# Kernel tuning notes

Measured on AMD Instinct MI355X. Metric: run time of the kernel, lower is better.

## Reference

```python
import jax, jax.numpy as jnp
import numpy as np

EPS = 1e-5

def _ln(x):
    m = jnp.mean(x, axis=-1, keepdims=True)
    v = jnp.mean((x - m) ** 2, axis=-1, keepdims=True)
    return (x - m) / jnp.sqrt(v + EPS)

def setup_inputs() -> dict:
    key = jax.random.key(0)
    ks = jax.random.split(key, 6)
    B, S, E, H = 2, 2048, 1024, 16
    sd = 1.0 / np.sqrt(E)
    x = jax.random.normal(ks[0], (B, S, E), dtype=jnp.float32)
    w_in = jax.random.normal(ks[1], (3 * E, E), dtype=jnp.float32) * sd
    w_out = jax.random.normal(ks[2], (E, E), dtype=jnp.float32) * sd
    w_fc = jax.random.normal(ks[3], (4 * E, E), dtype=jnp.float32) * sd
    b_fc = jnp.zeros((4 * E,), dtype=jnp.float32)
    w_proj = jax.random.normal(ks[4], (E, 4 * E), dtype=jnp.float32) * (1.0 / np.sqrt(4 * E))
    b_proj = jnp.zeros((E,), dtype=jnp.float32)
    return {"x": x, "w_in": w_in, "w_out": w_out, "w_fc": w_fc,
            "b_fc": b_fc, "w_proj": w_proj, "b_proj": b_proj}

def reference(x, w_in, w_out, w_fc, b_fc, w_proj, b_proj):
    B, S, E = x.shape
    H = 16
    D = E // H
    h = _ln(x)
    qkv = h @ w_in.T                      # [B,S,3E]
    q, k, v = jnp.split(qkv, 3, axis=-1)
    q = q.reshape(B, S, H, D)
    k = k.reshape(B, S, H, D)
    v = v.reshape(B, S, H, D)
    scale = 1.0 / np.sqrt(D)
    scores = jnp.einsum('bqhd,bkhd->bhqk', q, k) * scale  # [B,H,S,S]
    causal = jnp.tril(jnp.ones((S, S), dtype=bool))
    scores = jnp.where(causal, scores, -jnp.inf)
    attn = jax.nn.softmax(scores, axis=-1)
    o = jnp.einsum('bhqk,bkhd->bqhd', attn, v).reshape(B, S, E)
    attn_out = o @ w_out.T
    x2 = x + attn_out                      # residual 1
    h2 = _ln(x2)
    m = jax.nn.relu(h2 @ w_fc.T + b_fc)    # [B,S,4E]
    return (m @ w_proj.T + b_proj) + x2    # residual 2
```

## Files before the change

### kernel.cpp

```cpp
#include <hip/hip_runtime.h>
#include <stdint.h>

#define AS1 __attribute__((address_space(1)))
#define AS3 __attribute__((address_space(3)))

typedef __bf16 bf8_t __attribute__((ext_vector_type(8)));
typedef float f4_t __attribute__((ext_vector_type(4)));
typedef unsigned short ush;

__device__ __forceinline__ ush f2b(float f) {
  unsigned u = __builtin_bit_cast(unsigned, f);
  u += 0x7fffu + ((u >> 16) & 1u);
  return (ush)(u >> 16);
}
__device__ __forceinline__ void unpack8(uint4 u, float* dst) {
  unsigned a0 = u.x, a1 = u.y, a2 = u.z, a3 = u.w;
  dst[0] = __builtin_bit_cast(float, a0 << 16);
  dst[1] = __builtin_bit_cast(float, a0 & 0xffff0000u);
  dst[2] = __builtin_bit_cast(float, a1 << 16);
  dst[3] = __builtin_bit_cast(float, a1 & 0xffff0000u);
  dst[4] = __builtin_bit_cast(float, a2 << 16);
  dst[5] = __builtin_bit_cast(float, a2 & 0xffff0000u);
  dst[6] = __builtin_bit_cast(float, a3 << 16);
  dst[7] = __builtin_bit_cast(float, a3 & 0xffff0000u);
}

__global__ __launch_bounds__(256) void f2b_all(
    const float* __restrict__ w_in, const float* __restrict__ w_out,
    const float* __restrict__ w_fc, const float* __restrict__ w_proj,
    ush* __restrict__ o_in, ush* __restrict__ o_out,
    ush* __restrict__ o_fc, ush* __restrict__ o_proj) {
  const int blk = blockIdx.x;
  const float* src;
  ush* dst;
  int base;
  if (blk < 3072) { src = w_in; dst = o_in; base = blk; }
  else if (blk < 4096) { src = w_out; dst = o_out; base = blk - 3072; }
  else if (blk < 8192) { src = w_fc; dst = o_fc; base = blk - 4096; }
  else { src = w_proj; dst = o_proj; base = blk - 8192; }
  const int i = (base * 256 + threadIdx.x) * 4;
  float4 v = *(const float4*)(src + i);
  union { ush u[4]; uint2 d; } p;
  p.u[0] = f2b(v.x); p.u[1] = f2b(v.y); p.u[2] = f2b(v.z); p.u[3] = f2b(v.w);
  *(uint2*)(dst + i) = p.d;
}

__global__ __launch_bounds__(256) void ln_kernel(const float* __restrict__ x,
                                                 ush* __restrict__ out) {
  const int row = blockIdx.x, tid = threadIdx.x;
  const float* xr = x + (size_t)row * 1024;
  float4 v = ((const float4*)xr)[tid];
  float s = v.x + v.y + v.z + v.w;
  float q = v.x * v.x + v.y * v.y + v.z * v.z + v.w * v.w;
  for (int o = 32; o; o >>= 1) { s += __shfl_down(s, o); q += __shfl_down(q, o); }
  __shared__ float rs[4], rq[4];
  const int w = tid >> 6;
  if ((tid & 63) == 0) { rs[w] = s; rq[w] = q; }
  __syncthreads();
  s = rs[0] + rs[1] + rs[2] + rs[3];
  q = rq[0] + rq[1] + rq[2] + rq[3];
  const float mean = s * (1.0f / 1024.0f);
  const float var = q * (1.0f / 1024.0f) - mean * mean;
  const float rstd = rsqrtf(var + 1e-5f);
  union { ush u[4]; uint2 d; } p;
  p.u[0] = f2b((v.x - mean) * rstd);
  p.u[1] = f2b((v.y - mean) * rstd);
  p.u[2] = f2b((v.z - mean) * rstd);
  p.u[3] = f2b((v.w - mean) * rstd);
  *(uint2*)(out + (size_t)row * 1024 + tid * 4) = p.d;
}

template <int EPI>
__global__ __launch_bounds__(512, 2) void gemm8p(
    const ush* __restrict__ A, const ush* __restrict__ Bw,
    int M, int N, int K,
    const float* __restrict__ bias, const float* __restrict__ resid,
    float* __restrict__ outF, ush* __restrict__ outB) {
  __shared__ __align__(16) ush lds[65536];
  ush* const LA0 = lds;
  ush* const LA1 = lds + 16384;
  ush* const LB0 = lds + 32768;
  ush* const LB1 = lds + 49152;

  const int tid = threadIdx.x;
  const int wave = tid >> 6, lane = tid & 63;
  const int wm = wave >> 2, wn = wave & 3;
  const int l16 = lane & 15, quad = lane >> 4;
  const int sw = l16 & 7;
  const int bm = blockIdx.x, bn = blockIdx.y;
  const int bmrow = bm * 256, bnrow = bn * 256;
  const int KT = K >> 6;
  const int nit = KT >> 1;
  const int gcs = (((lane & 7) ^ ((lane >> 3) & 7)) << 3);

  auto stage = [&](const ush* __restrict__ gbase, int blkrow, ush* dstbase,
                   int t, int h) {
    const int kt = t & (KT - 1);
#pragma unroll
    for (int i2 = 0; i2 < 2; ++i2) {
      const int rr = h * 128 + (wave * 2 + i2) * 8 + (lane >> 3);
      const ush* g = gbase + (size_t)(blkrow + rr) * K + kt * 64 + gcs;
      __builtin_amdgcn_global_load_lds(
          (const AS1 void*)g,
          (AS3 void*)(dstbase + h * 8192 + (wave * 2 + i2) * 512), 16, 0, 0);
    }
  };

  f4_t acc[8][4];
#pragma unroll
  for (int i = 0; i < 8; ++i)
#pragma unroll
    for (int j = 0; j < 4; ++j) acc[i][j] = (f4_t){0.f, 0.f, 0.f, 0.f};

  stage(A, bmrow, LA0, 0, 0);
  stage(A, bmrow, LA0, 0, 1);
  stage(Bw, bnrow, LB0, 0, 0);
  stage(Bw, bnrow, LB0, 0, 1);
  stage(A, bmrow, LA1, 1, 0);
  asm volatile("s_waitcnt vmcnt(2)" ::: "memory");
  __builtin_amdgcn_s_barrier();

  bf8_t af[4][2], bf[2][2];

  for (int it = 0; it < nit; ++it) {
#pragma unroll
    for (int hf = 0; hf < 2; ++hf) {
      ush* const cA = hf ? LA1 : LA0;
      ush* const cB = hf ? LB1 : LB0;
#pragma unroll
      for (int sub = 0; sub < 4; ++sub) {
        const int p = hf * 4 + sub;
        if (sub == 0) {
#pragma unroll
          for (int m = 0; m < 4; ++m)
#pragma unroll
            for (int kk = 0; kk < 2; ++kk)
              af[m][kk] = *(const bf8_t*)&cA[(wm * 128 + m * 16 + l16) * 64 +
                                            (((kk * 4 + quad) ^ sw) << 3)];
#pragma unroll
          for (int n = 0; n < 2; ++n)
#pragma unroll
            for (int kk = 0; kk < 2; ++kk)
              bf[n][kk] = *(const bf8_t*)&cB[(wn * 64 + n * 16 + l16) * 64 +
                                            (((kk * 4 + quad) ^ sw) << 3)];
        } else if (sub == 1) {
#pragma unroll
          for (int n = 0; n < 2; ++n)
#pragma unroll
            for (int kk = 0; kk < 2; ++kk)
              bf[n][kk] = *(const bf8_t*)&cB[(wn * 64 + (2 + n) * 16 + l16) * 64 +
                                            (((kk * 4 + quad) ^ sw) << 3)];
        } else if (sub == 2) {
#pragma unroll
          for (int m = 0; m < 4; ++m)
#pragma unroll
            for (int kk = 0; kk < 2; ++kk)
              af[m][kk] = *(const bf8_t*)&cA[(wm * 128 + (4 + m) * 16 + l16) * 64 +
                                            (((kk * 4 + quad) ^ sw) << 3)];
#pragma unroll
          for (int n = 0; n < 2; ++n)
#pragma unroll
            for (int kk = 0; kk < 2; ++kk)
              bf[n][kk] = *(const bf8_t*)&cB[(wn * 64 + n * 16 + l16) * 64 +
                                            (((kk * 4 + quad) ^ sw) << 3)];
        } else {
#pragma unroll
          for (int n = 0; n < 2; ++n)
#pragma unroll
            for (int kk = 0; kk < 2; ++kk)
              bf[n][kk] = *(const bf8_t*)&cB[(wn * 64 + (2 + n) * 16 + l16) * 64 +
                                            (((kk * 4 + quad) ^ sw) << 3)];
        }
        if (p == 0) stage(A, bmrow, LA1, 2 * it + 1, 1);
        else if (p == 1) stage(Bw, bnrow, LB1, 2 * it + 1, 0);
        else if (p == 2) stage(Bw, bnrow, LB1, 2 * it + 1, 1);
        else if (p == 3) stage(A, bmrow, LA0, 2 * it + 2, 0);
        else if (p == 4) stage(A, bmrow, LA0, 2 * it + 2, 1);
        else if (p == 5) stage(Bw, bnrow, LB0, 2 * it + 2, 0);
        else if (p == 6) stage(Bw, bnrow, LB0, 2 * it + 2, 1);
        else stage(A, bmrow, LA1, 2 * it + 3, 0);
        if (sub == 3) asm volatile("s_waitcnt vmcnt(2)" ::: "memory");
        __builtin_amdgcn_s_barrier();
        asm volatile("s_waitcnt lgkmcnt(0)" ::: "memory");
        __builtin_amdgcn_sched_barrier(0);
        __builtin_amdgcn_s_setprio(1);
        const int mo = (sub >= 2) ? 4 : 0;
        const int no = (sub & 1) ? 2 : 0;
#pragma unroll
        for (int m = 0; m < 4; ++m)
#pragma unroll
          for (int n = 0; n < 2; ++n)
#pragma unroll
            for (int kk = 0; kk < 2; ++kk)
              acc[mo + m][no + n] = __builtin_amdgcn_mfma_f32_16x16x32_bf16(
                  af[m][kk], bf[n][kk], acc[mo + m][no + n], 0, 0, 0);
        __builtin_amdgcn_s_setprio(0);
        __builtin_amdgcn_s_barrier();
      }
    }
  }

  asm volatile("s_waitcnt vmcnt(0)" ::: "memory");
  __builtin_amdgcn_s_barrier();

  if (EPI == 0 || EPI == 2) {
    ush* eb = lds + wave * 8192;
    float bv[4];
    if (EPI == 2) {
#pragma unroll
      for (int ni = 0; ni < 4; ++ni) bv[ni] = bias[bn * 256 + wn * 64 + ni * 16 + l16];
    }
#pragma unroll
    for (int mi = 0; mi < 8; ++mi)
#pragma unroll
      for (int ni = 0; ni < 4; ++ni)
#pragma unroll
        for (int r = 0; r < 4; ++r) {
          float v = acc[mi][ni][r];
          if (EPI == 2) v = fmaxf(v + bv[ni], 0.0f);
          eb[(mi * 16 + quad * 4 + r) * 64 + ni * 16 + l16] = f2b(v);
        }
    asm volatile("s_waitcnt lgkmcnt(0)" ::: "memory");
#pragma unroll
    for (int j = 0; j < 16; ++j) {
      const int lr = j * 8 + (lane >> 3);
      const int c8 = (lane & 7) * 8;
      uint4 v = *(const uint4*)&eb[lr * 64 + c8];
      *(uint4*)(outB + (size_t)(bm * 256 + wm * 128 + lr) * N + bn * 256 +
                wn * 64 + c8) = v;
    }
  } else {
#pragma unroll
    for (int mi = 0; mi < 8; ++mi)
#pragma unroll
      for (int ni = 0; ni < 4; ++ni) {
        const int gm0 = bm * 256 + wm * 128 + mi * 16 + quad * 4;
        const int gn = bn * 256 + wn * 64 + ni * 16 + l16;
        const float bv = (EPI == 3) ? bias[gn] : 0.0f;
#pragma unroll
        for (int r = 0; r < 4; ++r) {
          const size_t idx = (size_t)(gm0 + r) * N + gn;
          outF[idx] = acc[mi][ni][r] + bv + resid[idx];
        }
      }
  }
}

template <int EPI, int BM, int MINW>
__global__ __launch_bounds__(256, MINW) void gemm_bt(
    const ush* __restrict__ A, const ush* __restrict__ Bw,
    int M, int N, int K,
    const float* __restrict__ bias, const float* __restrict__ resid,
    float* __restrict__ outF, ush* __restrict__ outB) {
  constexpr int MI = BM / 32;
  constexpr int NCH = (BM + 128) / 16;
  constexpr int PC = NCH / 4;
  constexpr int ASZ = BM * 32;
  __shared__ ush lds[2 * ASZ + 2 * 4096];
  const int tid = threadIdx.x;
  const int wave = tid >> 6, lane = tid & 63;
  const int bm = blockIdx.x, bn = blockIdx.y;
  const int wm = (wave & 1) * (BM / 2), wn = (wave >> 1) * 64;
  const int l16 = lane & 15, quad = lane >> 4;
  const int srow = lane >> 2;
  const int scol = (lane & 3) * 8;

  const ush* Abase = A + (size_t)(bm * BM) * K;
  const ush* Bbase = Bw + (size_t)(bn * 128) * K;

  f4_t acc[MI][4];
#pragma unroll
  for (int i = 0; i < MI; ++i)
#pragma unroll
    for (int j = 0; j < 4; ++j) acc[i][j] = (f4_t){0.f, 0.f, 0.f, 0.f};

  const int kiters = K >> 5;

  auto stage = [&](int k0, int buf) {
    const int kk = k0 * 32;
#pragma unroll
    for (int i = 0; i < PC; ++i) {
      const int c = wave * PC + i;
      if (c < BM / 16) {
        const ush* ga = Abase + (size_t)(c * 16 + srow) * K + kk + scol;
        __builtin_amdgcn_global_load_lds((const AS1 void*)ga,
                                         (AS3 void*)(lds + buf * ASZ + c * 512), 16, 0, 0);
      } else {
        const int c2 = c - BM / 16;
        const ush* gb = Bbase + (size_t)(c2 * 16 + srow) * K + kk + scol;
        __builtin_amdgcn_global_load_lds(
            (const AS1 void*)gb, (AS3 void*)(lds + 2 * ASZ + buf * 4096 + c2 * 512), 16, 0, 0);
      }
    }
  };

  stage(0, 0);
  __syncthreads();
  for (int k0 = 0; k0 < kiters; ++k0) {
    const int cur = k0 & 1;
    if (k0 + 1 < kiters) stage(k0 + 1, cur ^ 1);
    bf8_t af[MI], bfr[4];
#pragma unroll
    for (int mi = 0; mi < MI; ++mi)
      af[mi] = *(const bf8_t*)&lds[cur * ASZ + (wm + mi * 16 + l16) * 32 + quad * 8];
#pragma unroll
    for (int ni = 0; ni < 4; ++ni)
      bfr[ni] = *(const bf8_t*)&lds[2 * ASZ + cur * 4096 + (wn + ni * 16 + l16) * 32 + quad * 8];
#pragma unroll
    for (int mi = 0; mi < MI; ++mi)
#pragma unroll
      for (int ni = 0; ni < 4; ++ni)
        acc[mi][ni] =
            __builtin_amdgcn_mfma_f32_16x16x32_bf16(af[mi], bfr[ni], acc[mi][ni], 0, 0, 0);
    __syncthreads();
  }

  if (EPI == 0 || EPI == 2) {
    ush* eb = lds + wave * ASZ;
#pragma unroll
    for (int mi = 0; mi < MI; ++mi)
#pragma unroll
      for (int ni = 0; ni < 4; ++ni) {
        const int gn = bn * 128 + wn + ni * 16 + l16;
        const float bv = (EPI == 2) ? bias[gn] : 0.0f;
#pragma unroll
        for (int r = 0; r < 4; ++r) {
          float v = acc[mi][ni][r] + bv;
          if (EPI == 2) v = fmaxf(v, 0.0f);
          eb[(mi * 16 + quad * 4 + r) * 64 + ni * 16 + l16] = f2b(v);
        }
      }
#pragma unroll
    for (int j = 0; j < BM / 16; ++j) {
      const int lr = j * 8 + (lane >> 3);
      const int c8 = (lane & 7) * 8;
      uint4 v = *(const uint4*)&eb[lr * 64 + c8];
      *(uint4*)(outB + (size_t)(bm * BM + wm + lr) * N + bn * 128 + wn + c8) = v;
    }
  } else {
#pragma unroll
    for (int mi = 0; mi < MI; ++mi) {
#pragma unroll
      for (int ni = 0; ni < 4; ++ni) {
        const int gm0 = bm * BM + wm + mi * 16 + quad * 4;
        const int gn = bn * 128 + wn + ni * 16 + l16;
        const float bv = (EPI == 3) ? bias[gn] : 0.0f;
#pragma unroll
        for (int r = 0; r < 4; ++r) {
          const size_t idx = (size_t)(gm0 + r) * N + gn;
          outF[idx] = acc[mi][ni][r] + bv + resid[idx];
        }
      }
    }
  }
}

__global__ __launch_bounds__(256) void pack_kv(const ush* __restrict__ qkv,
                                               ush* __restrict__ Kp,
                                               ush* __restrict__ Vp) {
  const int lin = blockIdx.x;
  const int kt = lin & 31, h = (lin >> 5) & 15, b = lin >> 9;
  const int tid = threadIdx.x;
  __shared__ ush Vs[64 * 72];
  const size_t rowbase = (size_t)(b * 2048 + kt * 64) * 3072 + h * 64;
  ush* Kt = Kp + (size_t)lin * 4096;
  ush* Vt = Vp + (size_t)lin * 4096;

  const int r0 = tid >> 3, cin = tid & 7;
#pragma unroll
  for (int it = 0; it < 2; ++it) {
    const int r = r0 + it * 32;
    uint4 ku = *(const uint4*)(qkv + rowbase + (size_t)r * 3072 + 1024 + cin * 8);
    float f[8]; unpack8(ku, f);
    union { ush us[8]; uint4 v; } pk;
#pragma unroll
    for (int j = 0; j < 8; ++j) pk.us[j] = f2b(f[j] * 0.125f);
    *(uint4*)(Kt + (size_t)(r * 8 + (cin ^ (r & 7))) * 8) = pk.v;
    uint4 vu = *(const uint4*)(qkv + rowbase + (size_t)r * 3072 + 2048 + cin * 8);
    *(uint4*)&Vs[r * 72 + cin * 8] = vu;
  }
  __syncthreads();
#pragma unroll
  for (int oc2 = 0; oc2 < 2; ++oc2) {
    const int oc = tid * 2 + oc2;
    const int d = oc >> 3, c = oc & 7;
    const int k0 = 8 * (c ^ (d & 7));
    union { ush us[8]; uint4 v; } pk;
#pragma unroll
    for (int j = 0; j < 8; ++j) pk.us[j] = Vs[(k0 + j) * 72 + d];
    *(uint4*)(Vt + (size_t)oc * 8) = pk.v;
  }
}

__global__ __launch_bounds__(256, 4) void attn_kernel(const ush* __restrict__ qkv,
                                                      const ush* __restrict__ Kp,
                                                      const ush* __restrict__ Vp,
                                                      ush* __restrict__ o) {
  const int lin = blockIdx.x;
  const int b = lin & 1, h = (lin >> 1) & 15, tq = lin >> 5;
  const int tid = threadIdx.x;
  const int wave = tid >> 6, lane = tid & 63;
  const int l15 = lane & 15, quad = lane >> 4;

  __shared__ __align__(16) ush Ks[64 * 64];
  __shared__ __align__(16) ush Vt[64 * 64];
  __shared__ __align__(16) ush Ps[64 * 72];

  bf8_t qf[2];
  {
    const int qrow = b * 2048 + tq * 64 + wave * 16 + l15;
#pragma unroll
    for (int s = 0; s < 2; ++s) {
      union { uint4 u; bf8_t v; } pk;
      pk.u = *(const uint4*)(qkv + (size_t)qrow * 3072 + h * 64 + s * 32 + quad * 8);
      qf[s] = pk.v;
    }
  }

  float m_s = -1e30f, l_s = 0.f;
  f4_t O[4];
#pragma unroll
  for (int j = 0; j < 4; ++j) O[j] = (f4_t){0.f, 0.f, 0.f, 0.f};

  const int qw0 = tq * 64 + wave * 16;
  const int swz = (l15 & 7) * 8;
  const size_t tile0 = (size_t)((b * 16 + h) * 32) * 4096;

  for (int kt = 0; kt <= tq; ++kt) {
    __syncthreads();
    const ush* Ktile = Kp + tile0 + (size_t)kt * 4096;
    const ush* Vtile = Vp + tile0 + (size_t)kt * 4096;
#pragma unroll
    for (int i = 0; i < 2; ++i) {
      const int seg = wave * 2 + i;
      __builtin_amdgcn_global_load_lds((const AS1 void*)(Ktile + seg * 512 + lane * 8),
                                       (AS3 void*)(Ks + seg * 512), 16, 0, 0);
      __builtin_amdgcn_global_load_lds((const AS1 void*)(Vtile + seg * 512 + lane * 8),
                                       (AS3 void*)(Vt + seg * 512), 16, 0, 0);
    }
    __syncthreads();

    f4_t S[4];
#pragma unroll
    for (int mi = 0; mi < 4; ++mi) S[mi] = (f4_t){0.f, 0.f, 0.f, 0.f};
#pragma unroll
    for (int s = 0; s < 2; ++s)
#pragma unroll
      for (int mi = 0; mi < 4; ++mi) {
        bf8_t kf = *(const bf8_t*)&Ks[(mi * 16 + l15) * 64 + (((4 * s + quad) * 8) ^ swz)];
        S[mi] = __builtin_amdgcn_mfma_f32_16x16x32_bf16(kf, qf[s], S[mi], 0, 0, 0);
      }

    if (kt == tq) {
#pragma unroll
      for (int mi = 0; mi < 4; ++mi)
#pragma unroll
        for (int r = 0; r < 4; ++r) {
          const int kg = kt * 64 + mi * 16 + quad * 4 + r;
          const int qg = qw0 + l15;
          if (kg > qg) S[mi][r] = -1e30f;
        }
    }

    float mx = -1e30f;
#pragma unroll
    for (int mi = 0; mi < 4; ++mi)
#pragma unroll
      for (int r = 0; r < 4; ++r) mx = fmaxf(mx, S[mi][r]);
    mx = fmaxf(mx, __shfl_xor(mx, 16));
    mx = fmaxf(mx, __shfl_xor(mx, 32));
    const float mn = fmaxf(m_s, mx);
    const float alpha = __expf(m_s - mn);
    float sum = 0.f;
#pragma unroll
    for (int mi = 0; mi < 4; ++mi)
#pragma unroll
      for (int r = 0; r < 4; ++r) {
        const float p = __expf(S[mi][r] - mn);
        S[mi][r] = p;
        sum += p;
      }
    sum += __shfl_xor(sum, 16);
    sum += __shfl_xor(sum, 32);
    m_s = mn;
    l_s = l_s * alpha + sum;
#pragma unroll
    for (int mi = 0; mi < 4; ++mi) {
      uint2 w2;
      w2.x = (unsigned)f2b(S[mi][0]) | ((unsigned)f2b(S[mi][1]) << 16);
      w2.y = (unsigned)f2b(S[mi][2]) | ((unsigned)f2b(S[mi][3]) << 16);
      *(uint2*)&Ps[(wave * 16 + l15) * 72 + mi * 16 + quad * 4] = w2;
    }

    bf8_t pf[2], vf[4][2];
#pragma unroll
    for (int s = 0; s < 2; ++s)
      pf[s] = *(const bf8_t*)&Ps[(wave * 16 + l15) * 72 + s * 32 + quad * 8];
#pragma unroll
    for (int n4 = 0; n4 < 4; ++n4)
#pragma unroll
      for (int s = 0; s < 2; ++s)
        vf[n4][s] = *(const bf8_t*)&Vt[(n4 * 16 + l15) * 64 + (((4 * s + quad) * 8) ^ swz)];
    float ar[4];
#pragma unroll
    for (int r = 0; r < 4; ++r) ar[r] = __shfl(alpha, quad * 4 + r);
#pragma unroll
    for (int n4 = 0; n4 < 4; ++n4) {
#pragma unroll
      for (int r = 0; r < 4; ++r) O[n4][r] *= ar[r];
#pragma unroll
      for (int s = 0; s < 2; ++s)
        O[n4] = __builtin_amdgcn_mfma_f32_16x16x32_bf16(pf[s], vf[n4][s], O[n4], 0, 0, 0);
    }
  }

  const float rc = 1.0f / l_s;
  float rr[4];
#pragma unroll
  for (int r = 0; r < 4; ++r) rr[r] = __shfl(rc, quad * 4 + r);
#pragma unroll
  for (int n4 = 0; n4 < 4; ++n4)
#pragma unroll
    for (int r = 0; r < 4; ++r) {
      const int qg = tq * 64 + wave * 16 + quad * 4 + r;
      o[(size_t)(b * 2048 + qg) * 1024 + h * 64 + n4 * 16 + l15] = f2b(O[n4][r] * rr[r]);
    }
}

extern "C" void kernel_launch(void* const* d_in, const int* in_sizes, int n_in,
                              void* d_out, int out_size, void* d_ws, size_t ws_size,
                              hipStream_t stream) {
  const float* x = (const float*)d_in[0];
  const float* w_in = (const float*)d_in[1];
  const float* w_out = (const float*)d_in[2];
  const float* w_fc = (const float*)d_in[3];
  const float* b_fc = (const float*)d_in[4];
  const float* w_proj = (const float*)d_in[5];
  const float* b_proj = (const float*)d_in[6];
  float* out = (float*)d_out;

  char* ws = (char*)d_ws;
  ush* w_in_b = (ush*)(ws);
  ush* w_out_b = (ush*)(ws + 6291456);
  ush* w_fc_b = (ush*)(ws + 8388608);
  ush* w_proj_b = (ush*)(ws + 16777216);
  ush* h_b = (ush*)(ws + 25165824);
  float* x2 = (float*)(ws + 33554432);
  ush* qkv_b = (ush*)(ws + 50331648);
  ush* o_b = (ush*)(ws + 75497472);
  ush* m_b = (ush*)(ws + 50331648);
  ush* Kp = (ush*)(ws + 83886080);
  ush* Vp = (ush*)(ws + 92274688);

  f2b_all<<<12288, 256, 0, stream>>>(w_in, w_out, w_fc, w_proj,
                                     w_in_b, w_out_b, w_fc_b, w_proj_b);

  ln_kernel<<<4096, 256, 0, stream>>>(x, h_b);

  gemm8p<0><<<dim3(16, 12), 512, 0, stream>>>(
      h_b, w_in_b, 4096, 3072, 1024, nullptr, nullptr, nullptr, qkv_b);

  pack_kv<<<1024, 256, 0, stream>>>(qkv_b, Kp, Vp);

  attn_kernel<<<1024, 256, 0, stream>>>(qkv_b, Kp, Vp, o_b);

  gemm_bt<1, 64, 4><<<dim3(64, 8), 256, 0, stream>>>(
      o_b, w_out_b, 4096, 1024, 1024, nullptr, x, x2, nullptr);

  ln_kernel<<<4096, 256, 0, stream>>>(x2, h_b);

  gemm8p<2><<<dim3(16, 16), 512, 0, stream>>>(
      h_b, w_fc_b, 4096, 4096, 1024, b_fc, nullptr, nullptr, m_b);

  gemm_bt<3, 64, 4><<<dim3(64, 8), 256, 0, stream>>>(
      m_b, w_proj_b, 4096, 1024, 4096, b_proj, x2, out, nullptr);
}
```

Baseline: 328.7 us.

## Split-K the MLP down-projection over the 256x256 GEMM with a separate reduction

Replaces the 64-row gemm_bt kernel for the final projection (K=4096) with the larger 256x256-tile gemm8p kernel split four ways along K via blockIdx.z. Each split writes a bf16 partial, and a new reduce4 kernel sums the four partials and adds the bias and residual. The goal is to use the more efficient big-tile GEMM while keeping enough blocks (256) to fill the device. The cost is an extra kernel launch, an extra pass over the partials in memory, and bf16 rounding of the partial sums, which loses precision. The workspace layout is reshuffled so the partials can reuse the weight-conversion region.

After: 310.2 us. 1.06x faster.

```diff
diff --git a/kernel.cpp b/kernel.cpp
--- a/kernel.cpp
+++ b/kernel.cpp
@@ -73,7 +73,7 @@
 template <int EPI>
 __global__ __launch_bounds__(512, 2) void gemm8p(
     const ush* __restrict__ A, const ush* __restrict__ Bw,
-    int M, int N, int K,
+    int M, int N, int K, int lda, int ldb,
     const float* __restrict__ bias, const float* __restrict__ resid,
     float* __restrict__ outF, ush* __restrict__ outB) {
   __shared__ __align__(16) ush lds[65536];
@@ -89,17 +89,18 @@
   const int sw = l16 & 7;
   const int bm = blockIdx.x, bn = blockIdx.y;
   const int bmrow = bm * 256, bnrow = bn * 256;
+  const size_t kbase = (size_t)blockIdx.z * (size_t)K;
   const int KT = K >> 6;
   const int nit = KT >> 1;
   const int gcs = (((lane & 7) ^ ((lane >> 3) & 7)) << 3);
 
-  auto stage = [&](const ush* __restrict__ gbase, int blkrow, ush* dstbase,
-                   int t, int h) {
+  auto stage = [&](const ush* __restrict__ gbase, int blkrow, int ld,
+                   ush* dstbase, int t, int h) {
     const int kt = t & (KT - 1);
 #pragma unroll
     for (int i2 = 0; i2 < 2; ++i2) {
       const int rr = h * 128 + (wave * 2 + i2) * 8 + (lane >> 3);
-      const ush* g = gbase + (size_t)(blkrow + rr) * K + kt * 64 + gcs;
+      const ush* g = gbase + (size_t)(blkrow + rr) * ld + kbase + kt * 64 + gcs;
       __builtin_amdgcn_global_load_lds(
           (const AS1 void*)g,
           (AS3 void*)(dstbase + h * 8192 + (wave * 2 + i2) * 512), 16, 0, 0);
@@ -112,11 +113,11 @@
 #pragma unroll
     for (int j = 0; j < 4; ++j) acc[i][j] = (f4_t){0.f, 0.f, 0.f, 0.f};
 
-  stage(A, bmrow, LA0, 0, 0);
-  stage(A, bmrow, LA0, 0, 1);
-  stage(Bw, bnrow, LB0, 0, 0);
-  stage(Bw, bnrow, LB0, 0, 1);
-  stage(A, bmrow, LA1, 1, 0);
+  stage(A, bmrow, lda, LA0, 0, 0);
+  stage(A, bmrow, lda, LA0, 0, 1);
+  stage(Bw, bnrow, ldb, LB0, 0, 0);
+  stage(Bw, bnrow, ldb, LB0, 0, 1);
+  stage(A, bmrow, lda, LA1, 1, 0);
   asm volatile("s_waitcnt vmcnt(2)" ::: "memory");
   __builtin_amdgcn_s_barrier();
 
@@ -171,14 +172,14 @@
               bf[n][kk] = *(const bf8_t*)&cB[(wn * 64 + (2 + n) * 16 + l16) * 64 +
                                             (((kk * 4 + quad) ^ sw) << 3)];
         }
-        if (p == 0) stage(A, bmrow, LA1, 2 * it + 1, 1);
-        else if (p == 1) stage(Bw, bnrow, LB1, 2 * it + 1, 0);
-        else if (p == 2) stage(Bw, bnrow, LB1, 2 * it + 1, 1);
-        else if (p == 3) stage(A, bmrow, LA0, 2 * it + 2, 0);
-        else if (p == 4) stage(A, bmrow, LA0, 2 * it + 2, 1);
-        else if (p == 5) stage(Bw, bnrow, LB0, 2 * it + 2, 0);
-        else if (p == 6) stage(Bw, bnrow, LB0, 2 * it + 2, 1);
-        else stage(A, bmrow, LA1, 2 * it + 3, 0);
+        if (p == 0) stage(A, bmrow, lda, LA1, 2 * it + 1, 1);
+        else if (p == 1) stage(Bw, bnrow, ldb, LB1, 2 * it + 1, 0);
+        else if (p == 2) stage(Bw, bnrow, ldb, LB1, 2 * it + 1, 1);
+        else if (p == 3) stage(A, bmrow, lda, LA0, 2 * it + 2, 0);
+        else if (p == 4) stage(A, bmrow, lda, LA0, 2 * it + 2, 1);
+        else if (p == 5) stage(Bw, bnrow, ldb, LB0, 2 * it + 2, 0);
+        else if (p == 6) stage(Bw, bnrow, ldb, LB0, 2 * it + 2, 1);
+        else stage(A, bmrow, lda, LA1, 2 * it + 3, 0);
         if (sub == 3) asm volatile("s_waitcnt vmcnt(2)" ::: "memory");
         __builtin_amdgcn_s_barrier();
         asm volatile("s_waitcnt lgkmcnt(0)" ::: "memory");
@@ -204,6 +205,7 @@
   __builtin_amdgcn_s_barrier();
 
   if (EPI == 0 || EPI == 2) {
+    ush* outBz = outB + (size_t)blockIdx.z * ((size_t)M * N);
     ush* eb = lds + wave * 8192;
     float bv[4];
     if (EPI == 2) {
@@ -226,7 +228,7 @@
       const int lr = j * 8 + (lane >> 3);
       const int c8 = (lane & 7) * 8;
       uint4 v = *(const uint4*)&eb[lr * 64 + c8];
-      *(uint4*)(outB + (size_t)(bm * 256 + wm * 128 + lr) * N + bn * 256 +
+      *(uint4*)(outBz + (size_t)(bm * 256 + wm * 128 + lr) * N + bn * 256 +
                 wn * 64 + c8) = v;
     }
   } else {
@@ -244,6 +246,30 @@
         }
       }
   }
+}
+
+__global__ __launch_bounds__(256) void reduce4(const ush* __restrict__ p,
+                                               const float* __restrict__ bias,
+                                               const float* __restrict__ resid,
+                                               float* __restrict__ out) {
+  const size_t i = ((size_t)blockIdx.x * 256 + threadIdx.x) * 8;
+  const int col = (int)(i & 1023);
+  float acc[8];
+  float4 r0 = *(const float4*)(resid + i);
+  float4 r1 = *(const float4*)(resid + i + 4);
+  acc[0] = r0.x + bias[col + 0]; acc[1] = r0.y + bias[col + 1];
+  acc[2] = r0.z + bias[col + 2]; acc[3] = r0.w + bias[col + 3];
+  acc[4] = r1.x + bias[col + 4]; acc[5] = r1.y + bias[col + 5];
+  acc[6] = r1.z + bias[col + 6]; acc[7] = r1.w + bias[col + 7];
+#pragma unroll
+  for (int z = 0; z < 4; ++z) {
+    uint4 u = *(const uint4*)(p + (size_t)z * 4194304 + i);
+    float f[8]; unpack8(u, f);
+#pragma unroll
+    for (int j = 0; j < 8; ++j) acc[j] += f[j];
+  }
+  *(float4*)(out + i) = *(float4*)acc;
+  *(float4*)(out + i + 4) = *(float4*)(acc + 4);
 }
 
 template <int EPI, int BM, int MINW>
@@ -542,15 +568,16 @@
   char* ws = (char*)d_ws;
   ush* w_in_b = (ush*)(ws);
   ush* w_out_b = (ush*)(ws + 6291456);
-  ush* w_fc_b = (ush*)(ws + 8388608);
-  ush* w_proj_b = (ush*)(ws + 16777216);
-  ush* h_b = (ush*)(ws + 25165824);
-  float* x2 = (float*)(ws + 33554432);
-  ush* qkv_b = (ush*)(ws + 50331648);
-  ush* o_b = (ush*)(ws + 75497472);
-  ush* m_b = (ush*)(ws + 50331648);
-  ush* Kp = (ush*)(ws + 83886080);
-  ush* Vp = (ush*)(ws + 92274688);
+  ush* h_b = (ush*)(ws + 8388608);
+  ush* Kp = (ush*)(ws + 16777216);
+  ush* Vp = (ush*)(ws + 25165824);
+  ush* Pp = (ush*)(ws);
+  ush* w_fc_b = (ush*)(ws + 33554432);
+  ush* w_proj_b = (ush*)(ws + 41943040);
+  float* x2 = (float*)(ws + 50331648);
+  ush* qkv_b = (ush*)(ws + 67108864);
+  ush* m_b = (ush*)(ws + 67108864);
+  ush* o_b = (ush*)(ws + 92274688);
 
   f2b_all<<<12288, 256, 0, stream>>>(w_in, w_out, w_fc, w_proj,
                                      w_in_b, w_out_b, w_fc_b, w_proj_b);
@@ -558,7 +585,7 @@
   ln_kernel<<<4096, 256, 0, stream>>>(x, h_b);
 
   gemm8p<0><<<dim3(16, 12), 512, 0, stream>>>(
-      h_b, w_in_b, 4096, 3072, 1024, nullptr, nullptr, nullptr, qkv_b);
+      h_b, w_in_b, 4096, 3072, 1024, 1024, 1024, nullptr, nullptr, nullptr, qkv_b);
 
   pack_kv<<<1024, 256, 0, stream>>>(qkv_b, Kp, Vp);
 
@@ -570,8 +597,10 @@
   ln_kernel<<<4096, 256, 0, stream>>>(x2, h_b);
 
   gemm8p<2><<<dim3(16, 16), 512, 0, stream>>>(
-      h_b, w_fc_b, 4096, 4096, 1024, b_fc, nullptr, nullptr, m_b);
-
-  gemm_bt<3, 64, 4><<<dim3(64, 8), 256, 0, stream>>>(
-      m_b, w_proj_b, 4096, 1024, 4096, b_proj, x2, out, nullptr);
-}
+      h_b, w_fc_b, 4096, 4096, 1024, 1024, 1024, b_fc, nullptr, nullptr, m_b);
+
+  gemm8p<0><<<dim3(16, 4, 4), 512, 0, stream>>>(
+      m_b, w_proj_b, 4096, 1024, 1024, 4096, 4096, nullptr, nullptr, nullptr, Pp);
+
+  reduce4<<<2048, 256, 0, stream>>>(Pp, b_proj, x2, out);
+}
```
